# Kernel optimization log

Hardware: AMD Instinct MI355X
Metric: run time of the kernel (lower is better)

Reference implementation:

```python
import jax, jax.numpy as jnp
import numpy as np

CHANNELS = 8
IN_CHANNELS = 8
MASK_OUT_STRIDE = 4
WEIGHT_NUMS = [(IN_CHANNELS + 2) * CHANNELS, CHANNELS * CHANNELS, CHANNELS * 1]
BIAS_NUMS = [CHANNELS, CHANNELS, 1]
SOI = jnp.array([8.0, 16.0, 32.0, 64.0, 128.0], dtype=jnp.float32)
EPS = 1e-5


def compute_locations(h, w, stride):
    # (x, y) center of each stride-sized cell, row-major (y outer, x inner)
    sx = jnp.arange(w, dtype=jnp.float32) * stride + stride // 2
    sy = jnp.arange(h, dtype=jnp.float32) * stride + stride // 2
    yy, xx = jnp.meshgrid(sy, sx, indexing='ij')
    return jnp.stack([xx.reshape(-1), yy.reshape(-1)], axis=-1)  # [H*W, 2]


def aligned_bilinear(t, factor):
    # Matches AdelaiDet aligned_bilinear: replicate-pad right/bottom, bilinear
    # upsample align_corners=True to (f*h+1, f*w+1), replicate-pad top/left by
    # f//2, crop to (f*h, f*w).
    if factor == 1:
        return t
    n, c, h, w = t.shape
    t = jnp.pad(t, ((0, 0), (0, 0), (0, 1), (0, 1)), mode='edge')  # [n,c,h+1,w+1]
    oh, ow = factor * h + 1, factor * w + 1
    ys = jnp.arange(oh, dtype=jnp.float32) / factor  # align_corners mapping
    xs = jnp.arange(ow, dtype=jnp.float32) / factor
    y0 = jnp.floor(ys).astype(jnp.int32)
    x0 = jnp.floor(xs).astype(jnp.int32)
    y1 = jnp.minimum(y0 + 1, h)
    x1 = jnp.minimum(x0 + 1, w)
    wy = (ys - y0.astype(jnp.float32)).astype(t.dtype)
    wx = (xs - x0.astype(jnp.float32)).astype(t.dtype)
    ty = t[:, :, y0, :] * (1.0 - wy)[None, None, :, None] + t[:, :, y1, :] * wy[None, None, :, None]
    out = ty[:, :, :, x0] * (1.0 - wx) + ty[:, :, :, x1] * wx
    p = factor // 2
    out = jnp.pad(out, ((0, 0), (0, 0), (p, 0), (p, 0)), mode='edge')
    return out[:, :, :oh - 1, :ow - 1]


def parse_dynamic_params(params):
    n = params.shape[0]
    splits = jnp.split(params, np.cumsum(WEIGHT_NUMS + BIAS_NUMS)[:-1], axis=1)
    w0 = splits[0].reshape(n, CHANNELS, IN_CHANNELS + 2)
    w1 = splits[1].reshape(n, CHANNELS, CHANNELS)
    w2 = splits[2].reshape(n, 1, CHANNELS)
    b0 = splits[3].reshape(n, CHANNELS)
    b1 = splits[4].reshape(n, CHANNELS)
    b2 = splits[5].reshape(n, 1)
    return (w0, w1, w2), (b0, b1, b2)


def setup_inputs() -> dict:
    key = jax.random.key(0)
    ks = jax.random.split(key, 6)
    N, H, W = 2, 100, 136
    n_inst = 500
    return {
        'mask_feats': jax.random.normal(ks[0], (N, IN_CHANNELS, H, W), dtype=jnp.float32),
        'mask_head_params': jax.random.normal(ks[1], (n_inst, 169), dtype=jnp.float32),
        'locations_inst': jax.random.uniform(ks[2], (n_inst, 2), dtype=jnp.float32),
        'gt_bitmasks': jax.random.uniform(ks[3], (n_inst, 1, 2 * H, 2 * W), dtype=jnp.float32),
        'im_inds': jax.random.randint(ks[4], (n_inst,), 0, N, dtype=jnp.int64 if jax.config.jax_enable_x64 else jnp.int32),
        'fpn_levels': jax.random.randint(ks[5], (n_inst,), 0, 5, dtype=jnp.int64 if jax.config.jax_enable_x64 else jnp.int32),
        'mask_feat_stride': 8,
    }


def reference(mask_feats, mask_head_params, locations_inst, gt_bitmasks, im_inds, fpn_levels, mask_feat_stride):
    N, Cin, H, W = mask_feats.shape
    n = mask_head_params.shape[0]
    # relative coordinates, normalized by per-instance size-of-interest
    locs = compute_locations(H, W, mask_feat_stride)                 # [HW, 2]
    rel = locations_inst[:, None, :] - locs[None, :, :]              # [n, HW, 2]
    rel = jnp.transpose(rel, (0, 2, 1))                              # [n, 2, HW]
    soi = SOI[fpn_levels]                                            # [n]
    rel = (rel / soi[:, None, None]).astype(mask_feats.dtype)
    feats = mask_feats[im_inds].reshape(n, Cin, H * W)               # gather per instance
    x = jnp.concatenate([rel, feats], axis=1)                        # [n, Cin+2, HW]
    # per-instance 1x1 conv stack == batched small GEMMs
    (w0, w1, w2), (b0, b1, b2) = parse_dynamic_params(mask_head_params)
    x = jax.nn.relu(jnp.einsum('nci,nip->ncp', w0, x) + b0[:, :, None])
    x = jax.nn.relu(jnp.einsum('nci,nip->ncp', w1, x) + b1[:, :, None])
    x = jnp.einsum('nci,nip->ncp', w2, x) + b2[:, :, None]           # [n, 1, HW]
    logits = x.reshape(n, 1, H, W)
    logits = aligned_bilinear(logits, mask_feat_stride // MASK_OUT_STRIDE)
    scores = jax.nn.sigmoid(logits)                                  # [n, 1, 2H, 2W]
    # dice loss
    xs = scores.reshape(n, -1)
    t = gt_bitmasks.reshape(n, -1)
    inter = jnp.sum(xs * t, axis=1)
    union = jnp.sum(xs * xs, axis=1) + jnp.sum(t * t, axis=1) + EPS
    loss = 1.0 - 2.0 * inter / union
    return jnp.mean(loss)
```

## Files before the change

kernel.cpp:

```cpp
#include <hip/hip_runtime.h>
#include <hip/hip_bf16.h>
#include <math.h>

#define CIN      8
#define H_IN     100
#define W_IN     136
#define NPIX     (H_IN * W_IN)
#define OH       (2 * H_IN)
#define OW       (2 * W_IN)
#define ONPIX    (OH * OW)
#define NPARAMS  169
#define EPSV     1e-5f
#define NSLICE   4
#define PAIRS_PER_SLICE 25
#define KGROUPS  34
#define TASKS    (PAIRS_PER_SLICE * KGROUPS)


__device__ __forceinline__ float sigmoidf_fast(float x) {
    float e = __expf(-x);
    return __builtin_amdgcn_rcpf(1.f + e);
}

__global__ __launch_bounds__(256, 2)
void mask_head_fused(const float* __restrict__ mask_feats,
                     const float* __restrict__ params,
                     const float* __restrict__ locs,
                     const float* __restrict__ gt,
                     const int*   __restrict__ im_inds,
                     const int*   __restrict__ fpn_levels,
                     float*       __restrict__ partials)
{
    const int inst  = blockIdx.x >> 2;
    const int slice = blockIdx.x & 3;
    const int tid   = threadIdx.x;

    const int r_start = (slice == 0) ? 0 : 25 * slice - 1;
    const int r_end   = 25 * slice + 24;
    const int nrows   = r_end - r_start + 1;
    const int npx     = nrows * W_IN;

    __shared__ float s_par[NPARAMS];
    __shared__ float s_logit[26 * W_IN];
    __shared__ float s_red[12];

    if (tid < NPARAMS) s_par[tid] = params[inst * NPARAMS + tid];

    const int   im  = im_inds[inst];
    const int   lvl = fpn_levels[inst];
    const float inv_soi = exp2f(-(float)(3 + lvl));
    const float lx = locs[inst * 2 + 0];
    const float ly = locs[inst * 2 + 1];

    __syncthreads();

    const float* feat = mask_feats + (size_t)im * (CIN * NPIX);
    const int goff = r_start * W_IN;

    #pragma unroll 1
    for (int base = 0; base < 26 * W_IN; base += 1024) {
        const int p0 = base + tid;
        float in[10][4];
        #pragma unroll
        for (int k = 0; k < 4; ++k) {
            int p  = p0 + (k << 8);
            int pc = p < npx ? p : npx - 1;
            int r  = pc / W_IN;
            int x  = pc - r * W_IN;
            int y  = r_start + r;
            in[0][k] = (lx - (float)(x * 8 + 4)) * inv_soi;
            in[1][k] = (ly - (float)(y * 8 + 4)) * inv_soi;
            int gp = goff + pc;
            #pragma unroll
            for (int c = 0; c < CIN; ++c)
                in[2 + c][k] = feat[c * NPIX + gp];
        }

        float h0[8][4];
        #pragma unroll
        for (int o = 0; o < 8; ++o) {
            float b = s_par[152 + o];
            float a0 = b, a1 = b, a2 = b, a3 = b;
            #pragma unroll
            for (int i = 0; i < 10; ++i) {
                float w = s_par[o * 10 + i];
                a0 = fmaf(w, in[i][0], a0);
                a1 = fmaf(w, in[i][1], a1);
                a2 = fmaf(w, in[i][2], a2);
                a3 = fmaf(w, in[i][3], a3);
            }
            h0[o][0] = fmaxf(a0, 0.f);
            h0[o][1] = fmaxf(a1, 0.f);
            h0[o][2] = fmaxf(a2, 0.f);
            h0[o][3] = fmaxf(a3, 0.f);
        }

        float h1[8][4];
        #pragma unroll
        for (int o = 0; o < 8; ++o) {
            float b = s_par[160 + o];
            float a0 = b, a1 = b, a2 = b, a3 = b;
            #pragma unroll
            for (int i = 0; i < 8; ++i) {
                float w = s_par[80 + o * 8 + i];
                a0 = fmaf(w, h0[i][0], a0);
                a1 = fmaf(w, h0[i][1], a1);
                a2 = fmaf(w, h0[i][2], a2);
                a3 = fmaf(w, h0[i][3], a3);
            }
            h1[o][0] = fmaxf(a0, 0.f);
            h1[o][1] = fmaxf(a1, 0.f);
            h1[o][2] = fmaxf(a2, 0.f);
            h1[o][3] = fmaxf(a3, 0.f);
        }

        float b2 = s_par[168];
        float o0 = b2, o1 = b2, o2 = b2, o3 = b2;
        #pragma unroll
        for (int i = 0; i < 8; ++i) {
            float w = s_par[144 + i];
            o0 = fmaf(w, h1[i][0], o0);
            o1 = fmaf(w, h1[i][1], o1);
            o2 = fmaf(w, h1[i][2], o2);
            o3 = fmaf(w, h1[i][3], o3);
        }
        float outv[4] = {o0, o1, o2, o3};
        #pragma unroll
        for (int k = 0; k < 4; ++k) {
            int p = p0 + (k << 8);
            if (p < npx) s_logit[p] = outv[k];
        }
    }

    __syncthreads();

    float inter = 0.f, ssum = 0.f, tsum = 0.f;
    const float* gtp = gt + (size_t)inst * ONPIX;
    const int pair_base = 25 * slice;

    #pragma unroll 1
    for (int base = 0; base < TASKS; base += 256) {
        const int task = base + tid;
        if (task < TASKS) {
            const int pl = task / KGROUPS;
            const int k  = task - pl * KGROUPS;
            const int pg = pair_base + pl;
            const int er = pg - r_start;
            const int pr = (pg > 0 ? pg - 1 : 0) - r_start;
            const float* E = s_logit + er * W_IN;
            const float* P = s_logit + pr * W_IN;
            const int c0  = 4 * k;
            const int cm1 = (k > 0) ? c0 - 1 : 0;

            const float4 e4 = *(const float4*)(E + c0);
            const float  em = E[cm1];
            const float4 p4 = *(const float4*)(P + c0);
            const float  pm = P[cm1];

            const float* g0 = gtp + (size_t)(2 * pg) * OW + 8 * k;
            const float4 ga = *(const float4*)(g0);
            const float4 gb = *(const float4*)(g0 + 4);
            const float4 gc = *(const float4*)(g0 + OW);
            const float4 gd = *(const float4*)(g0 + OW + 4);

            const float ecur[4] = {e4.x, e4.y, e4.z, e4.w};
            const float pcur[4] = {p4.x, p4.y, p4.z, p4.w};
            const float gav[8]  = {ga.x, ga.y, ga.z, ga.w, gb.x, gb.y, gb.z, gb.w};
            const float gex[8]  = {gc.x, gc.y, gc.z, gc.w, gd.x, gd.y, gd.z, gd.w};

            float Se_prev = em;
            float Sa_prev = 0.5f * (em + pm);
            #pragma unroll
            for (int j = 0; j < 4; ++j) {
                const float Se = ecur[j];
                const float Sa = 0.5f * (ecur[j] + pcur[j]);
                {
                    float s = sigmoidf_fast(0.5f * (Sa_prev + Sa));
                    float t = gav[2 * j];
                    inter = fmaf(s, t, inter); ssum = fmaf(s, s, ssum); tsum = fmaf(t, t, tsum);
                    s = sigmoidf_fast(Sa);
                    t = gav[2 * j + 1];
                    inter = fmaf(s, t, inter); ssum = fmaf(s, s, ssum); tsum = fmaf(t, t, tsum);
                }
                {
                    float s = sigmoidf_fast(0.5f * (Se_prev + Se));
                    float t = gex[2 * j];
                    inter = fmaf(s, t, inter); ssum = fmaf(s, s, ssum); tsum = fmaf(t, t, tsum);
                    s = sigmoidf_fast(Se);
                    t = gex[2 * j + 1];
                    inter = fmaf(s, t, inter); ssum = fmaf(s, s, ssum); tsum = fmaf(t, t, tsum);
                }
                Se_prev = Se;
                Sa_prev = Sa;
            }
        }
    }

    #pragma unroll
    for (int off = 32; off > 0; off >>= 1) {
        inter += __shfl_down(inter, off, 64);
        ssum  += __shfl_down(ssum,  off, 64);
        tsum  += __shfl_down(tsum,  off, 64);
    }
    const int wid = tid >> 6;
    if ((tid & 63) == 0) {
        s_red[wid * 3 + 0] = inter;
        s_red[wid * 3 + 1] = ssum;
        s_red[wid * 3 + 2] = tsum;
    }
    __syncthreads();
    if (tid == 0) {
        float I = 0.f, S = 0.f, T = 0.f;
        #pragma unroll
        for (int w = 0; w < 4; ++w) {
            I += s_red[w * 3 + 0];
            S += s_red[w * 3 + 1];
            T += s_red[w * 3 + 2];
        }
        partials[blockIdx.x * 3 + 0] = I;
        partials[blockIdx.x * 3 + 1] = S;
        partials[blockIdx.x * 3 + 2] = T;
    }
}

__global__ __launch_bounds__(512)
void loss_mean_kernel(const float* __restrict__ partials, float* __restrict__ out, int n)
{
    __shared__ float s_red[8];
    float v = 0.f;
    for (int i = threadIdx.x; i < n; i += 512) {
        float I = 0.f, S = 0.f, T = 0.f;
        #pragma unroll
        for (int s = 0; s < NSLICE; ++s) {
            const float* p = partials + (size_t)(i * NSLICE + s) * 3;
            I += p[0];
            S += p[1];
            T += p[2];
        }
        v += 1.f - 2.f * I / (S + T + EPSV);
    }
    #pragma unroll
    for (int off = 32; off > 0; off >>= 1) v += __shfl_down(v, off, 64);
    const int wid = threadIdx.x >> 6;
    if ((threadIdx.x & 63) == 0) s_red[wid] = v;
    __syncthreads();
    if (threadIdx.x == 0) {
        float s = 0.f;
        #pragma unroll
        for (int w = 0; w < 8; ++w) s += s_red[w];
        out[0] = s / (float)n;
    }
}

extern "C" void kernel_launch(void* const* d_in, const int* in_sizes, int n_in,
                              void* d_out, int out_size, void* d_ws, size_t ws_size,
                              hipStream_t stream)
{
    const float* mask_feats = (const float*)d_in[0];
    const float* params     = (const float*)d_in[1];
    const float* locs       = (const float*)d_in[2];
    const float* gt         = (const float*)d_in[3];
    const int*   im_inds    = (const int*)d_in[4];
    const int*   fpn_levels = (const int*)d_in[5];

    const int n = in_sizes[4];
    float* partials = (float*)d_ws;

    mask_head_fused<<<n * NSLICE, 256, 0, stream>>>(mask_feats, params, locs, gt,
                                                    im_inds, fpn_levels, partials);
    loss_mean_kernel<<<1, 512, 0, stream>>>(partials, (float*)d_out, n);
}
```

Before: 204.4 us.

## Read dynamic weights via scalar loads, halve per-thread pixels, raise occupancy

Dynamic conv weights are no longer staged in shared memory. They are read directly from global memory through a uniform pointer, which the compiler can serve with scalar loads. This drops the initial barrier and per-FMA LDS reads. Each thread now processes 2 pixels per iteration instead of 4 to cut register pressure, and launch bounds ask for 3 blocks per CU. The trade-off is less ILP per thread and more loop iterations, plus reliance on scalar cache hits for the weights.

```diff
diff --git a/kernel.cpp b/kernel.cpp
--- a/kernel.cpp
+++ b/kernel.cpp
@@ -12,9 +12,9 @@
 #define NPARAMS  169
 #define EPSV     1e-5f
 #define NSLICE   4
-#define PAIRS_PER_SLICE 25
 #define KGROUPS  34
-#define TASKS    (PAIRS_PER_SLICE * KGROUPS)
+#define TASKS    (25 * KGROUPS)
+#define NITER_A  7
 
 
 __device__ __forceinline__ float sigmoidf_fast(float x) {
@@ -22,7 +22,7 @@
     return __builtin_amdgcn_rcpf(1.f + e);
 }
 
-__global__ __launch_bounds__(256, 2)
+__global__ __launch_bounds__(256, 3)
 void mask_head_fused(const float* __restrict__ mask_feats,
                      const float* __restrict__ params,
                      const float* __restrict__ locs,
@@ -36,15 +36,13 @@
     const int tid   = threadIdx.x;
 
     const int r_start = (slice == 0) ? 0 : 25 * slice - 1;
-    const int r_end   = 25 * slice + 24;
-    const int nrows   = r_end - r_start + 1;
+    const int nrows   = (slice == 0) ? 25 : 26;
     const int npx     = nrows * W_IN;
 
-    __shared__ float s_par[NPARAMS];
     __shared__ float s_logit[26 * W_IN];
     __shared__ float s_red[12];
 
-    if (tid < NPARAMS) s_par[tid] = params[inst * NPARAMS + tid];
+    const float* __restrict__ wp = params + (size_t)inst * NPARAMS;
 
     const int   im  = im_inds[inst];
     const int   lvl = fpn_levels[inst];
@@ -52,84 +50,73 @@
     const float lx = locs[inst * 2 + 0];
     const float ly = locs[inst * 2 + 1];
 
-    __syncthreads();
-
     const float* feat = mask_feats + (size_t)im * (CIN * NPIX);
     const int goff = r_start * W_IN;
 
     #pragma unroll 1
-    for (int base = 0; base < 26 * W_IN; base += 1024) {
-        const int p0 = base + tid;
-        float in[10][4];
-        #pragma unroll
-        for (int k = 0; k < 4; ++k) {
-            int p  = p0 + (k << 8);
-            int pc = p < npx ? p : npx - 1;
-            int r  = pc / W_IN;
-            int x  = pc - r * W_IN;
-            int y  = r_start + r;
-            in[0][k] = (lx - (float)(x * 8 + 4)) * inv_soi;
-            in[1][k] = (ly - (float)(y * 8 + 4)) * inv_soi;
-            int gp = goff + pc;
-            #pragma unroll
-            for (int c = 0; c < CIN; ++c)
-                in[2 + c][k] = feat[c * NPIX + gp];
-        }
-
-        float h0[8][4];
+    for (int it = 0; it < NITER_A; ++it) {
+        const int p0 = it * 512 + tid;
+        const int p1 = p0 + 256;
+        const int pc0 = p0 < npx ? p0 : npx - 1;
+        const int pc1 = p1 < npx ? p1 : npx - 1;
+        const int r0 = pc0 / W_IN;
+        const int x0 = pc0 - r0 * W_IN;
+        const int r1 = pc1 / W_IN;
+        const int x1 = pc1 - r1 * W_IN;
+
+        float in[10][2];
+        in[0][0] = (lx - (float)(x0 * 8 + 4)) * inv_soi;
+        in[1][0] = (ly - (float)((r_start + r0) * 8 + 4)) * inv_soi;
+        in[0][1] = (lx - (float)(x1 * 8 + 4)) * inv_soi;
+        in[1][1] = (ly - (float)((r_start + r1) * 8 + 4)) * inv_soi;
+        const int g0 = goff + pc0;
+        const int g1 = goff + pc1;
+        #pragma unroll
+        for (int c = 0; c < CIN; ++c) {
+            in[2 + c][0] = feat[c * NPIX + g0];
+            in[2 + c][1] = feat[c * NPIX + g1];
+        }
+
+        float h0[8][2];
         #pragma unroll
         for (int o = 0; o < 8; ++o) {
-            float b = s_par[152 + o];
-            float a0 = b, a1 = b, a2 = b, a3 = b;
+            const float b = wp[152 + o];
+            float a0 = b, a1 = b;
             #pragma unroll
             for (int i = 0; i < 10; ++i) {
-                float w = s_par[o * 10 + i];
+                const float w = wp[o * 10 + i];
                 a0 = fmaf(w, in[i][0], a0);
                 a1 = fmaf(w, in[i][1], a1);
-                a2 = fmaf(w, in[i][2], a2);
-                a3 = fmaf(w, in[i][3], a3);
             }
             h0[o][0] = fmaxf(a0, 0.f);
             h0[o][1] = fmaxf(a1, 0.f);
-            h0[o][2] = fmaxf(a2, 0.f);
-            h0[o][3] = fmaxf(a3, 0.f);
-        }
-
-        float h1[8][4];
+        }
+
+        float h1[8][2];
         #pragma unroll
         for (int o = 0; o < 8; ++o) {
-            float b = s_par[160 + o];
-            float a0 = b, a1 = b, a2 = b, a3 = b;
+            const float b = wp[160 + o];
+            float a0 = b, a1 = b;
             #pragma unroll
             for (int i = 0; i < 8; ++i) {
-                float w = s_par[80 + o * 8 + i];
+                const float w = wp[80 + o * 8 + i];
                 a0 = fmaf(w, h0[i][0], a0);
                 a1 = fmaf(w, h0[i][1], a1);
-                a2 = fmaf(w, h0[i][2], a2);
-                a3 = fmaf(w, h0[i][3], a3);
             }
             h1[o][0] = fmaxf(a0, 0.f);
             h1[o][1] = fmaxf(a1, 0.f);
-            h1[o][2] = fmaxf(a2, 0.f);
-            h1[o][3] = fmaxf(a3, 0.f);
-        }
-
-        float b2 = s_par[168];
-        float o0 = b2, o1 = b2, o2 = b2, o3 = b2;
+        }
+
+        const float b2 = wp[168];
+        float o0 = b2, o1 = b2;
         #pragma unroll
         for (int i = 0; i < 8; ++i) {
-            float w = s_par[144 + i];
+            const float w = wp[144 + i];
             o0 = fmaf(w, h1[i][0], o0);
             o1 = fmaf(w, h1[i][1], o1);
-            o2 = fmaf(w, h1[i][2], o2);
-            o3 = fmaf(w, h1[i][3], o3);
-        }
-        float outv[4] = {o0, o1, o2, o3};
-        #pragma unroll
-        for (int k = 0; k < 4; ++k) {
-            int p = p0 + (k << 8);
-            if (p < npx) s_logit[p] = outv[k];
-        }
+        }
+        if (p0 < npx) s_logit[p0] = o0;
+        if (p1 < npx) s_logit[p1] = o1;
     }
 
     __syncthreads();
```

Result: slower. 219.4 us (+7.3%).
